# Kernel optimization log

Hardware: AMD Instinct MI355X
Metric: run time of the kernel (lower is better)

## Reference

```python
import jax, jax.numpy as jnp
import numpy as np

BLADES = ['', '1', '2', '3', '12', '13', '23', '123']
GEO = (3, 0, 0)  # geometrical_def: 3 basis vectors squaring to +1
NB = 8  # multivector_length

def _sq(idx):
    if idx < GEO[0] + 1:
        return 1
    if idx < GEO[0] + GEO[1] + 1:
        return -1
    return 0

def _ga_mul(a, b):
    l1 = [int(c) for c in a]; l2 = [int(c) for c in b]
    s = 1; i1 = 0; i2 = 0; n = len(l1); out = []
    while i1 < len(l1) and i2 < len(l2):
        if l1[i1] == l2[i2]:
            if (n - 1) % 2 != 0:
                s = -s
            s *= _sq(l1[i1]); n -= 1; i1 += 1; i2 += 1
        elif l1[i1] > l2[i2]:
            if n % 2 != 0:
                s = -s
            out.append(l2[i2]); i2 += 1
        else:
            out.append(l1[i1]); n -= 1; i1 += 1
    out += l1[i1:] + l2[i2:]
    return s, ''.join(map(str, out))

def cayley_table():
    # T[i, j, k] = s such that blade_i * blade_j = s * blade_k
    T = np.zeros((NB, NB, NB), dtype=np.float32)
    for i in range(NB):
        for j in range(NB):
            s, idx = _ga_mul(BLADES[i], BLADES[j])
            T[i, j, BLADES.index(idx)] = s
    return jnp.asarray(T)

_CAYLEY = cayley_table()

def setup_inputs() -> dict:
    key = jax.random.key(0)
    k1, k2, k3 = jax.random.split(key, 3)
    BS, C_IN, UNITS = 512, 1024, 1024
    x = jax.random.normal(k1, (NB * BS, C_IN), dtype=jnp.float32)
    W = jax.random.normal(k2, (C_IN, NB * UNITS), dtype=jnp.float32) * (1.0 / np.sqrt(C_IN))
    bias = jax.random.normal(k3, (1, NB * UNITS), dtype=jnp.float32) * 0.02
    return {"input_tensor": x, "W": W, "bias": bias}

def reference(input_tensor, W, bias):
    M = input_tensor.shape[0] // NB   # per-blade batch size
    U = W.shape[1] // NB              # per-blade output channels
    y = input_tensor @ W              # (8M, 8U) dense linear op
    y = y.reshape(NB, M, NB * U)      # split along batch axis into blades i
    y = y.at[0].add(bias[0])          # BiasLayer applied to blade-0 split only
    y = y.reshape(NB, M, NB, U)       # split along channel axis into blades j
    # fused Cayley combine: out[k] = sum_{i,j} T[i,j,k] * y[i,:,j,:]
    out = jnp.einsum('imju,ijk->kmu', y, _CAYLEY)
    return out.reshape(NB * M, U)
```

## Files before the change

### kernel.cpp

```cpp
#include <hip/hip_runtime.h>
#include <stdint.h>

#define NBL 8
#define MBS 512
#define CIN 1024
#define UQ  1024

__device__ __constant__ int   c_xs0[8] = {0,1,1,0,4,2,2,4};
__device__ __constant__ int   c_xs1[8] = {3,5,5,3,7,6,6,7};
__device__ __constant__ float c_xc0[8] = {1,1,1,1,1,-1,1,-1};
__device__ __constant__ float c_xc1[8] = {1,-1,1,-1,1,1,1,1};
__device__ __constant__ float c_wc0[8] = {0.5f,0.5f,0.5f,0.5f,0.5f,-0.5f,0.5f,-0.5f};
__device__ __constant__ float c_wc1[8] = {0.5f,-0.5f,0.5f,-0.5f,0.5f,0.5f,0.5f,0.5f};
__device__ __constant__ int c_sa[8][4] = {
  {0,8,1,9},{0,4,1,5},{0,8,1,9},{0,4,1,5},
  {2,10,3,11},{2,6,3,7},{2,10,3,11},{2,6,3,7}};
__device__ __constant__ int c_sb[8][4] = {
  {0,4,2,6},{4,0,6,2},{1,5,3,7},{5,1,7,3},
  {0,4,2,6},{4,0,6,2},{1,5,3,7},{5,1,7,3}};
__device__ __constant__ int   c_eb0[8] = {0,4,1,2,1,2,0,4};
__device__ __constant__ float c_es0[8] = {1,1,1,-1,1,1,1,-1};
__device__ __constant__ int   c_eb1[8] = {3,7,5,6,5,6,3,7};
__device__ __constant__ float c_es1[8] = {1,1,-1,1,1,1,-1,1};

__device__ __constant__ int c_sigma[8][8] = {
  {0,1,2,3,4,5,6,7},{1,0,4,5,2,3,7,6},{2,4,0,6,1,7,3,5},{3,5,6,0,7,1,2,4},
  {4,2,1,7,0,6,5,3},{5,3,7,1,6,0,4,2},{6,7,3,2,5,4,0,1},{7,6,5,4,3,2,1,0}};
__device__ __constant__ int c_sg[8][8] = {
  {1,1,1,1,1,1,1,1},{1,1,1,1,1,1,1,1},{1,-1,1,1,-1,-1,1,-1},{1,-1,-1,1,1,-1,-1,1},
  {-1,1,-1,-1,1,1,-1,1},{-1,1,1,-1,-1,1,1,-1},{-1,-1,1,-1,1,-1,1,1},{-1,-1,1,-1,1,-1,1,1}};

typedef short bf16x8 __attribute__((ext_vector_type(8)));
typedef float f32x4 __attribute__((ext_vector_type(4)));

__device__ __forceinline__ uint32_t f2bf(float f) {
  uint32_t u = __float_as_uint(f);
  return (u + 0x7fffu + ((u >> 16) & 1u)) >> 16;
}
__device__ __forceinline__ uint32_t pk2(float lo, float hi) {
  return f2bf(lo) | (f2bf(hi) << 16);
}

__global__ void cvt_x_kernel(const float* __restrict__ x, uint4* __restrict__ xv) {
  __shared__ uint4 t16[32 * 33];
  const int tid = threadIdx.x;
  const int tx = tid & 31, ty = tid >> 5;
  const int v  = blockIdx.x >> 2;
  const int cb = blockIdx.x & 3;
  const int m0 = blockIdx.y * 32;
  const int s0 = c_xs0[v] * MBS, s1 = c_xs1[v] * MBS;
  const float c0 = c_xc0[v], c1 = c_xc1[v];
#pragma unroll
  for (int r = 0; r < 4; ++r) {
    const int m = m0 + ty + r * 8;
    const float* pa = x + (size_t)(s0 + m) * CIN + cb * 256 + tx * 8;
    const float* pb = x + (size_t)(s1 + m) * CIN + cb * 256 + tx * 8;
    float4 a0 = *(const float4*)pa, a1 = *(const float4*)(pa + 4);
    float4 b0 = *(const float4*)pb, b1 = *(const float4*)(pb + 4);
    float4 f0, f1;
    f0.x = c0*a0.x + c1*b0.x; f0.y = c0*a0.y + c1*b0.y;
    f0.z = c0*a0.z + c1*b0.z; f0.w = c0*a0.w + c1*b0.w;
    f1.x = c0*a1.x + c1*b1.x; f1.y = c0*a1.y + c1*b1.y;
    f1.z = c0*a1.z + c1*b1.z; f1.w = c0*a1.w + c1*b1.w;
    uint4 p;
    p.x = pk2(f0.x, f0.y); p.y = pk2(f0.z, f0.w);
    p.z = pk2(f1.x, f1.y); p.w = pk2(f1.z, f1.w);
    t16[tx * 33 + ty + r * 8] = p;
  }
  __syncthreads();
#pragma unroll
  for (int p = 0; p < 4; ++p) {
    const int slot = p * 256 + tid;
    const int cc = slot >> 5, mm = slot & 31;
    uint4 val = t16[cc * 33 + mm];
    const size_t o = (size_t)(v * 128 + cb * 32 + cc) * 512 + m0 + mm;
    xv[o] = val;
    if (v >= 4) {
      uint4 n;
      n.x = val.x ^ 0x80008000u; n.y = val.y ^ 0x80008000u;
      n.z = val.z ^ 0x80008000u; n.w = val.w ^ 0x80008000u;
      xv[o + (size_t)4 * 65536] = n;
    }
  }
}

__global__ void cvt_w_kernel(const float* __restrict__ w, uint4* __restrict__ wv) {
  __shared__ float ta[32][65], tb[32][65];
  const int tid = threadIdx.x;
  const int tx = tid & 63, ty = tid >> 6;
  const int v  = blockIdx.x >> 4;
  const int nb = blockIdx.x & 15;
  const int k0 = blockIdx.y * 32;
  const int s0c = c_xs0[v] * UQ + nb * 64;
  const int s1c = c_xs1[v] * UQ + nb * 64;
#pragma unroll
  for (int r = 0; r < 8; ++r) {
    const int kr = ty * 8 + r;
    ta[kr][tx] = w[(size_t)(k0 + kr) * 8192 + s0c + tx];
    tb[kr][tx] = w[(size_t)(k0 + kr) * 8192 + s1c + tx];
  }
  __syncthreads();
  {
    const int cc = tid >> 6;
    const int uu = tid & 63;
    const float c0 = c_wc0[v], c1 = c_wc1[v];
    float e[8];
#pragma unroll
    for (int q = 0; q < 8; ++q)
      e[q] = c0 * ta[cc * 8 + q][uu] + c1 * tb[cc * 8 + q][uu];
    uint4 o;
    o.x = pk2(e[0], e[1]); o.y = pk2(e[2], e[3]);
    o.z = pk2(e[4], e[5]); o.w = pk2(e[6], e[7]);
    wv[(size_t)(v * 128 + blockIdx.y * 4 + cc) * 1024 + nb * 64 + uu] = o;
  }
}

__global__ void bias_fill(const float* __restrict__ bias, float4* __restrict__ out) {
  int idx = blockIdx.x * 256 + threadIdx.x;
  int row = idx >> 8;
  int c4 = idx & 255;
  int k = row >> 9;
  out[idx] = ((const float4*)(bias + k * UQ))[c4];
}

__global__ void merge_kernel(float* out, const float* __restrict__ part,
                             const float* __restrict__ bias) {
  const int q4 = blockIdx.x * 256 + threadIdx.x;
  f32x4* o4 = (f32x4*)out;
  const f32x4* p4 = (const f32x4*)part;
  const f32x4* b4 = (const f32x4*)bias;
  f32x4 P[8];
#pragma unroll
  for (int d = 0; d < 8; ++d)
    P[d] = o4[d * 131072 + q4] + p4[d * 131072 + q4];
  const int u4 = q4 & 255;
  o4[0 * 131072 + q4] = P[0] + P[6] + b4[0 * 256 + u4];
  o4[1 * 131072 + q4] = P[2] + P[4] + b4[1 * 256 + u4];
  o4[2 * 131072 + q4] = P[5] - P[3] + b4[2 * 256 + u4];
  o4[3 * 131072 + q4] = P[0] - P[6] + b4[3 * 256 + u4];
  o4[4 * 131072 + q4] = P[1] - P[7] + b4[4 * 256 + u4];
  o4[5 * 131072 + q4] = P[4] - P[2] + b4[5 * 256 + u4];
  o4[6 * 131072 + q4] = P[3] + P[5] + b4[6 * 256 + u4];
  o4[7 * 131072 + q4] = P[1] + P[7] + b4[7 * 256 + u4];
}

#define BAR() do { asm volatile("s_barrier" ::: "memory");                    \
                   __builtin_amdgcn_sched_barrier(0); } while (0)
#define VMW(N) asm volatile("s_waitcnt vmcnt(" #N ")" ::: "memory")

template<int ATOMIC>
__global__ __launch_bounds__(256, 2) void ga_cplx(
    const uint16_t* __restrict__ xv, const uint16_t* __restrict__ wv,
    float* __restrict__ out, float* __restrict__ part) {
  __shared__ uint16_t lds[4][8192];

  const int tid  = threadIdx.x;
  const int bid  = blockIdx.x;
  const int s    = bid >> 8;
  const int d    = (bid >> 5) & 7;
  const int mt   = (bid >> 3) & 3;
  const int ut   = bid & 7;
  const int lane = tid & 63;
  const int wid  = tid >> 6;
  const int wr   = wid >> 1, wc = wid & 1;
  const int r15  = lane & 15, hi = lane >> 4;

  const uint16_t* aB0 = xv + (size_t)c_sa[d][s * 2 + 0] * 524288;
  const uint16_t* aB1 = xv + (size_t)c_sa[d][s * 2 + 1] * 524288;
  const uint16_t* bB0 = wv + (size_t)c_sb[d][s * 2 + 0] * 1048576;
  const uint16_t* bB1 = wv + (size_t)c_sb[d][s * 2 + 1] * 1048576;

  const int hc = tid >> 7;
  const size_t mrow8 = (size_t)(mt * 128 + (tid & 127)) * 8;
  const size_t urow8 = (size_t)(ut * 128 + (tid & 127)) * 8;

  f32x4 acc[4][4];
  const f32x4 z = {0.f, 0.f, 0.f, 0.f};
#pragma unroll
  for (int a = 0; a < 4; ++a)
#pragma unroll
    for (int b = 0; b < 4; ++b) acc[a][b] = z;

  auto stage = [&](int u) {
    const uint16_t* pa = (u & 32) ? aB1 : aB0;
    const uint16_t* pb = (u & 32) ? bB1 : bB0;
    const int c0 = (u & 31) << 2;
    uint16_t* la = lds[u & 3];
    uint16_t* lb = lds[u & 3] + 4096;
#pragma unroll
    for (int u2 = 0; u2 < 2; ++u2) {
      const int cc = c0 + u2 * 2 + hc;
      __builtin_amdgcn_global_load_lds(
          (const __attribute__((address_space(1))) uint32_t*)(pa + (size_t)cc * 4096 + mrow8),
          (__attribute__((address_space(3))) uint32_t*)(la + (u2 * 256 + tid) * 8), 16, 0, 0);
      __builtin_amdgcn_global_load_lds(
          (const __attribute__((address_space(1))) uint32_t*)(pb + (size_t)cc * 8192 + urow8),
          (__attribute__((address_space(3))) uint32_t*)(lb + (u2 * 256 + tid) * 8), 16, 0, 0);
    }
  };

#define READF(FA, FB, RB) {                                                   \
  const uint16_t* b_ = lds[(RB)];                                             \
  _Pragma("unroll")                                                           \
  for (int f = 0; f < 4; ++f)                                                 \
    FA[f] = *(const bf16x8*)(b_ + ((hi << 7) + wr * 64 + f * 16 + r15) * 8);  \
  _Pragma("unroll")                                                           \
  for (int g = 0; g < 4; ++g)                                                 \
    FB[g] = *(const bf16x8*)(b_ + 4096 + ((hi << 7) + wc * 64 + g * 16 + r15) * 8); \
}

#define ITER(T, CA, CB, LA, LB) {                                             \
  VMW(4);                                                                     \
  BAR();                                                                      \
  stage(((T) + 3 < 63) ? (T) + 3 : 63);                                       \
  READF(LA, LB, ((((T) + 1 < 63) ? (T) + 1 : 63) & 3));                       \
  __builtin_amdgcn_sched_barrier(0);                                          \
  __builtin_amdgcn_s_setprio(1);                                              \
  _Pragma("unroll")                                                           \
  for (int f = 0; f < 4; ++f)                                                 \
    _Pragma("unroll")                                                         \
    for (int g = 0; g < 4; ++g)                                               \
      acc[f][g] = __builtin_amdgcn_mfma_f32_16x16x32_bf16(                    \
          CA[f], CB[g], acc[f][g], 0, 0, 0);                                  \
  __builtin_amdgcn_s_setprio(0);                                              \
}

  bf16x8 fCa[4], fCb[4], fNa[4], fNb[4];

  stage(0); stage(1); stage(2);
  VMW(4);
  BAR();
  READF(fCa, fCb, 0);

  for (int t = 0; t < 64; t += 2) {
    ITER(t,     fCa, fCb, fNa, fNb);
    ITER(t + 1, fNa, fNb, fCa, fCb);
  }

  const int row0 = mt * 128 + wr * 64;
  const int col0 = ut * 128 + wc * 64;
  if constexpr (ATOMIC) {
    const int rb0 = c_eb0[d], rb1 = c_eb1[d];
    const float es0 = c_es0[d], es1 = c_es1[d];
#pragma unroll
    for (int g = 0; g < 4; ++g) {
      const int col = col0 + g * 16 + r15;
#pragma unroll
      for (int f = 0; f < 4; ++f) {
        const int r0 = row0 + f * 16 + hi * 4;
#pragma unroll
        for (int r = 0; r < 4; ++r) {
          const float val = acc[f][g][r];
          unsafeAtomicAdd(&out[(size_t)(rb0 * MBS + r0 + r) * UQ + col], es0 * val);
          unsafeAtomicAdd(&out[(size_t)(rb1 * MBS + r0 + r) * UQ + col], es1 * val);
        }
      }
    }
  } else {
    float* dst = (s ? part : out) + (size_t)d * 524288;
#pragma unroll
    for (int g = 0; g < 4; ++g) {
      const int col = col0 + g * 16 + r15;
#pragma unroll
      for (int f = 0; f < 4; ++f) {
        const int r0 = row0 + f * 16 + hi * 4;
#pragma unroll
        for (int r = 0; r < 4; ++r)
          dst[(size_t)(r0 + r) * UQ + col] = acc[f][g][r];
      }
    }
  }
}

__global__ void ga_naive(const float* __restrict__ x, const float* __restrict__ w,
                         const float* __restrict__ bias, float* __restrict__ out) {
  int col = blockIdx.x * 256 + threadIdx.x;
  int row = blockIdx.y;
  int k = row >> 9, m = row & 511;
  float acc = bias[k * UQ + col];
  for (int i = 0; i < 8; ++i) {
    int j = c_sigma[i][k];
    float s = (float)c_sg[i][k];
    const float* xr = x + (size_t)(i * MBS + m) * CIN;
    const float* wc = w + (size_t)j * UQ + col;
    float a = 0.f;
    for (int c = 0; c < CIN; ++c) a = fmaf(xr[c], wc[(size_t)c * (NBL * UQ)], a);
    acc = fmaf(s, a, acc);
  }
  out[(size_t)row * UQ + col] = acc;
}

extern "C" void kernel_launch(void* const* d_in, const int* in_sizes, int n_in,
                              void* d_out, int out_size, void* d_ws, size_t ws_size,
                              hipStream_t stream) {
  const float* x    = (const float*)d_in[0];
  const float* W    = (const float*)d_in[1];
  const float* bias = (const float*)d_in[2];
  float* out = (float*)d_out;

  const size_t needA = 44u * 1024u * 1024u;
  const size_t needB = 28u * 1024u * 1024u;
  if (ws_size < needB) {
    ga_naive<<<dim3(4, 4096), dim3(256), 0, stream>>>(x, W, bias, out);
    return;
  }

  uint16_t* xv = (uint16_t*)d_ws;
  uint16_t* wv = xv + 6291456;
  float* part  = (float*)((char*)d_ws + 29360128);

  cvt_x_kernel<<<dim3(32, 16), dim3(256), 0, stream>>>(x, (uint4*)xv);
  cvt_w_kernel<<<dim3(128, 32), dim3(256), 0, stream>>>(W, (uint4*)wv);

  if (ws_size >= needA) {
    ga_cplx<0><<<dim3(512), dim3(256), 0, stream>>>(xv, wv, out, part);
    merge_kernel<<<dim3(512), dim3(256), 0, stream>>>(out, part, bias);
  } else {
    bias_fill<<<dim3(4096), dim3(256), 0, stream>>>(bias, (float4*)out);
    ga_cplx<1><<<dim3(512), dim3(256), 0, stream>>>(xv, wv, out, nullptr);
  }
}
```

Baseline: 66.03 us.

## Pair blade combinations in conversion kernels and stagger LDS reads against MFMA per wave

The x and W conversion kernels now handle pairs of blade combinations (sum and difference of the same two source blades) in one block. Each source tile is read once and both bf16 outputs are written, which halves global reads in the preprocessing stage and halves the grid size. Separately, the GEMM main loop alternates ordering by wave parity: odd waves issue MFMAs before their LDS fragment reads, even waves read first. This is meant to interleave LDS traffic with matrix work across waves, at the cost of extra register pressure and possible scheduling hazards.

```diff
diff --git a/kernel.cpp b/kernel.cpp
--- a/kernel.cpp
+++ b/kernel.cpp
@@ -6,12 +6,14 @@
 #define CIN 1024
 #define UQ  1024
 
-__device__ __constant__ int   c_xs0[8] = {0,1,1,0,4,2,2,4};
-__device__ __constant__ int   c_xs1[8] = {3,5,5,3,7,6,6,7};
-__device__ __constant__ float c_xc0[8] = {1,1,1,1,1,-1,1,-1};
-__device__ __constant__ float c_xc1[8] = {1,-1,1,-1,1,1,1,1};
-__device__ __constant__ float c_wc0[8] = {0.5f,0.5f,0.5f,0.5f,0.5f,-0.5f,0.5f,-0.5f};
-__device__ __constant__ float c_wc1[8] = {0.5f,-0.5f,0.5f,-0.5f,0.5f,0.5f,0.5f,0.5f};
+__device__ __constant__ int   px_sA[4] = {0,1,4,2};
+__device__ __constant__ int   px_sB[4] = {3,5,7,6};
+__device__ __constant__ int   px_vA[4] = {0,1,4,5};
+__device__ __constant__ float px_cA0[4] = {1,1,1,-1};
+__device__ __constant__ float px_cA1[4] = {1,-1,1,1};
+__device__ __constant__ int   px_vB[4] = {3,2,7,6};
+__device__ __constant__ float px_cB0[4] = {1,1,-1,1};
+__device__ __constant__ float px_cB1[4] = {-1,1,1,1};
 __device__ __constant__ int c_sa[8][4] = {
   {0,8,1,9},{0,4,1,5},{0,8,1,9},{0,4,1,5},
   {2,10,3,11},{2,6,3,7},{2,10,3,11},{2,6,3,7}};
@@ -42,44 +44,53 @@
 }
 
 __global__ void cvt_x_kernel(const float* __restrict__ x, uint4* __restrict__ xv) {
-  __shared__ uint4 t16[32 * 33];
+  __shared__ uint4 tA[32 * 33], tB[32 * 33];
   const int tid = threadIdx.x;
   const int tx = tid & 31, ty = tid >> 5;
-  const int v  = blockIdx.x >> 2;
+  const int p  = blockIdx.x >> 2;
   const int cb = blockIdx.x & 3;
   const int m0 = blockIdx.y * 32;
-  const int s0 = c_xs0[v] * MBS, s1 = c_xs1[v] * MBS;
-  const float c0 = c_xc0[v], c1 = c_xc1[v];
+  const int sA = px_sA[p] * MBS, sB = px_sB[p] * MBS;
+  const float cA0 = px_cA0[p], cA1 = px_cA1[p];
+  const float cB0 = px_cB0[p], cB1 = px_cB1[p];
 #pragma unroll
   for (int r = 0; r < 4; ++r) {
     const int m = m0 + ty + r * 8;
-    const float* pa = x + (size_t)(s0 + m) * CIN + cb * 256 + tx * 8;
-    const float* pb = x + (size_t)(s1 + m) * CIN + cb * 256 + tx * 8;
+    const float* pa = x + (size_t)(sA + m) * CIN + cb * 256 + tx * 8;
+    const float* pb = x + (size_t)(sB + m) * CIN + cb * 256 + tx * 8;
     float4 a0 = *(const float4*)pa, a1 = *(const float4*)(pa + 4);
     float4 b0 = *(const float4*)pb, b1 = *(const float4*)(pb + 4);
-    float4 f0, f1;
-    f0.x = c0*a0.x + c1*b0.x; f0.y = c0*a0.y + c1*b0.y;
-    f0.z = c0*a0.z + c1*b0.z; f0.w = c0*a0.w + c1*b0.w;
-    f1.x = c0*a1.x + c1*b1.x; f1.y = c0*a1.y + c1*b1.y;
-    f1.z = c0*a1.z + c1*b1.z; f1.w = c0*a1.w + c1*b1.w;
-    uint4 p;
-    p.x = pk2(f0.x, f0.y); p.y = pk2(f0.z, f0.w);
-    p.z = pk2(f1.x, f1.y); p.w = pk2(f1.z, f1.w);
-    t16[tx * 33 + ty + r * 8] = p;
+    uint4 vA, vB;
+    vA.x = pk2(cA0*a0.x + cA1*b0.x, cA0*a0.y + cA1*b0.y);
+    vA.y = pk2(cA0*a0.z + cA1*b0.z, cA0*a0.w + cA1*b0.w);
+    vA.z = pk2(cA0*a1.x + cA1*b1.x, cA0*a1.y + cA1*b1.y);
+    vA.w = pk2(cA0*a1.z + cA1*b1.z, cA0*a1.w + cA1*b1.w);
+    vB.x = pk2(cB0*a0.x + cB1*b0.x, cB0*a0.y + cB1*b0.y);
+    vB.y = pk2(cB0*a0.z + cB1*b0.z, cB0*a0.w + cB1*b0.w);
+    vB.z = pk2(cB0*a1.x + cB1*b1.x, cB0*a1.y + cB1*b1.y);
+    vB.w = pk2(cB0*a1.z + cB1*b1.z, cB0*a1.w + cB1*b1.w);
+    tA[tx * 33 + ty + r * 8] = vA;
+    tB[tx * 33 + ty + r * 8] = vB;
   }
   __syncthreads();
-#pragma unroll
-  for (int p = 0; p < 4; ++p) {
-    const int slot = p * 256 + tid;
+  const int vA = px_vA[p], vB = px_vB[p];
+#pragma unroll
+  for (int ph = 0; ph < 4; ++ph) {
+    const int slot = ph * 256 + tid;
     const int cc = slot >> 5, mm = slot & 31;
-    uint4 val = t16[cc * 33 + mm];
-    const size_t o = (size_t)(v * 128 + cb * 32 + cc) * 512 + m0 + mm;
-    xv[o] = val;
-    if (v >= 4) {
-      uint4 n;
-      n.x = val.x ^ 0x80008000u; n.y = val.y ^ 0x80008000u;
-      n.z = val.z ^ 0x80008000u; n.w = val.w ^ 0x80008000u;
-      xv[o + (size_t)4 * 65536] = n;
+    const size_t off = (size_t)(cb * 32 + cc) * 512 + m0 + mm;
+    uint4 a = tA[cc * 33 + mm];
+    uint4 b = tB[cc * 33 + mm];
+    xv[(size_t)vA * 65536 + off] = a;
+    xv[(size_t)vB * 65536 + off] = b;
+    if (p >= 2) {
+      uint4 na, nb;
+      na.x = a.x ^ 0x80008000u; na.y = a.y ^ 0x80008000u;
+      na.z = a.z ^ 0x80008000u; na.w = a.w ^ 0x80008000u;
+      nb.x = b.x ^ 0x80008000u; nb.y = b.y ^ 0x80008000u;
+      nb.z = b.z ^ 0x80008000u; nb.w = b.w ^ 0x80008000u;
+      xv[(size_t)(vA + 4) * 65536 + off] = na;
+      xv[(size_t)(vB + 4) * 65536 + off] = nb;
     }
   }
 }
@@ -88,30 +99,38 @@
   __shared__ float ta[32][65], tb[32][65];
   const int tid = threadIdx.x;
   const int tx = tid & 63, ty = tid >> 6;
-  const int v  = blockIdx.x >> 4;
+  const int p  = blockIdx.x >> 4;
   const int nb = blockIdx.x & 15;
   const int k0 = blockIdx.y * 32;
-  const int s0c = c_xs0[v] * UQ + nb * 64;
-  const int s1c = c_xs1[v] * UQ + nb * 64;
+  const int sAc = px_sA[p] * UQ + nb * 64;
+  const int sBc = px_sB[p] * UQ + nb * 64;
 #pragma unroll
   for (int r = 0; r < 8; ++r) {
     const int kr = ty * 8 + r;
-    ta[kr][tx] = w[(size_t)(k0 + kr) * 8192 + s0c + tx];
-    tb[kr][tx] = w[(size_t)(k0 + kr) * 8192 + s1c + tx];
+    ta[kr][tx] = w[(size_t)(k0 + kr) * 8192 + sAc + tx];
+    tb[kr][tx] = w[(size_t)(k0 + kr) * 8192 + sBc + tx];
   }
   __syncthreads();
   {
     const int cc = tid >> 6;
     const int uu = tid & 63;
-    const float c0 = c_wc0[v], c1 = c_wc1[v];
-    float e[8];
-#pragma unroll
-    for (int q = 0; q < 8; ++q)
-      e[q] = c0 * ta[cc * 8 + q][uu] + c1 * tb[cc * 8 + q][uu];
-    uint4 o;
-    o.x = pk2(e[0], e[1]); o.y = pk2(e[2], e[3]);
-    o.z = pk2(e[4], e[5]); o.w = pk2(e[6], e[7]);
-    wv[(size_t)(v * 128 + blockIdx.y * 4 + cc) * 1024 + nb * 64 + uu] = o;
+    const float cA0 = 0.5f * px_cA0[p], cA1 = 0.5f * px_cA1[p];
+    const float cB0 = 0.5f * px_cB0[p], cB1 = 0.5f * px_cB1[p];
+    float eA[8], eB[8];
+#pragma unroll
+    for (int q = 0; q < 8; ++q) {
+      const float a = ta[cc * 8 + q][uu], b = tb[cc * 8 + q][uu];
+      eA[q] = cA0 * a + cA1 * b;
+      eB[q] = cB0 * a + cB1 * b;
+    }
+    uint4 oA, oB;
+    oA.x = pk2(eA[0], eA[1]); oA.y = pk2(eA[2], eA[3]);
+    oA.z = pk2(eA[4], eA[5]); oA.w = pk2(eA[6], eA[7]);
+    oB.x = pk2(eB[0], eB[1]); oB.y = pk2(eB[2], eB[3]);
+    oB.z = pk2(eB[4], eB[5]); oB.w = pk2(eB[6], eB[7]);
+    const size_t off = (size_t)(blockIdx.y * 4 + cc) * 1024 + nb * 64 + uu;
+    wv[(size_t)px_vA[p] * 131072 + off] = oA;
+    wv[(size_t)px_vB[p] * 131072 + off] = oB;
   }
 }
 
@@ -209,12 +228,7 @@
     FB[g] = *(const bf16x8*)(b_ + 4096 + ((hi << 7) + wc * 64 + g * 16 + r15) * 8); \
 }
 
-#define ITER(T, CA, CB, LA, LB) {                                             \
-  VMW(4);                                                                     \
-  BAR();                                                                      \
-  stage(((T) + 3 < 63) ? (T) + 3 : 63);                                       \
-  READF(LA, LB, ((((T) + 1 < 63) ? (T) + 1 : 63) & 3));                       \
-  __builtin_amdgcn_sched_barrier(0);                                          \
+#define MFMA16(CA, CB) {                                                      \
   __builtin_amdgcn_s_setprio(1);                                              \
   _Pragma("unroll")                                                           \
   for (int f = 0; f < 4; ++f)                                                 \
@@ -223,6 +237,23 @@
       acc[f][g] = __builtin_amdgcn_mfma_f32_16x16x32_bf16(                    \
           CA[f], CB[g], acc[f][g], 0, 0, 0);                                  \
   __builtin_amdgcn_s_setprio(0);                                              \
+}
+
+#define ITER(T, CA, CB, LA, LB) {                                             \
+  VMW(4);                                                                     \
+  BAR();                                                                      \
+  stage(((T) + 3 < 63) ? (T) + 3 : 63);                                       \
+  const int rb_ = (((T) + 1 < 63) ? (T) + 1 : 63) & 3;                        \
+  if (wid & 1) {                                                              \
+    __builtin_amdgcn_sched_barrier(0);                                        \
+    MFMA16(CA, CB);                                                           \
+    __builtin_amdgcn_sched_barrier(0);                                        \
+    READF(LA, LB, rb_);                                                       \
+  } else {                                                                    \
+    READF(LA, LB, rb_);                                                       \
+    __builtin_amdgcn_sched_barrier(0);                                        \
+    MFMA16(CA, CB);                                                           \
+  }                                                                           \
 }
 
   bf16x8 fCa[4], fCb[4], fNa[4], fNb[4];
@@ -309,8 +340,8 @@
   uint16_t* wv = xv + 6291456;
   float* part  = (float*)((char*)d_ws + 29360128);
 
-  cvt_x_kernel<<<dim3(32, 16), dim3(256), 0, stream>>>(x, (uint4*)xv);
-  cvt_w_kernel<<<dim3(128, 32), dim3(256), 0, stream>>>(W, (uint4*)wv);
+  cvt_x_kernel<<<dim3(16, 16), dim3(256), 0, stream>>>(x, (uint4*)xv);
+  cvt_w_kernel<<<dim3(64, 32), dim3(256), 0, stream>>>(W, (uint4*)wv);
 
   if (ws_size >= needA) {
     ga_cplx<0><<<dim3(512), dim3(256), 0, stream>>>(xv, wv, out, part);
```

Result: no change. 66.26 us (+0.4%).
